# Kernel tuning notes

Measured on AMD Instinct MI355X. Metric: run time of the kernel, lower is better.

The kernel has to match this reference:

```python
import jax, jax.numpy as jnp
import numpy as np

KAPPA = 0.1
U0 = 1.0
LATT = (32, 32, 32, 32)  # (Lx, Ly, Lz, Lt)


def _gamma_matrices(dtype=jnp.complex64):
    g = np.zeros((4, 4, 4), dtype=np.complex64)
    g[0] = np.array([[0, 0, 0, 1j], [0, 0, 1j, 0], [0, -1j, 0, 0], [-1j, 0, 0, 0]])
    g[1] = np.array([[0, 0, 0, -1], [0, 0, 1, 0], [0, 1, 0, 0], [-1, 0, 0, 0]])
    g[2] = np.array([[0, 0, 1j, 0], [0, 0, 0, -1j], [-1j, 0, 0, 0], [0, 1j, 0, 0]])
    g[3] = np.array([[0, 0, 1, 0], [0, 0, 0, 1], [1, 0, 0, 0], [0, 1, 0, 0]])
    return jnp.asarray(g, dtype=dtype)


def setup_inputs() -> dict:
    key = jax.random.key(0)
    k1, k2, k3, k4 = jax.random.split(key, 4)
    Lx, Ly, Lz, Lt = LATT
    src_shape = (4, 3, Lt, Lz, Ly, Lx)        # [s, c, t, z, y, x]
    U_shape = (3, 3, 4, Lt, Lz, Ly, Lx)       # [C, c, d, t, z, y, x]
    return {
        "src_re": jax.random.normal(k1, src_shape, dtype=jnp.float32),
        "src_im": jax.random.normal(k2, src_shape, dtype=jnp.float32),
        "U_re": jax.random.normal(k3, U_shape, dtype=jnp.float32),
        "U_im": jax.random.normal(k4, U_shape, dtype=jnp.float32),
    }


def _wilson(src, U, kappa=KAPPA, u_0=U0):
    """Wilson-Dirac operator: dest = src - kappa/u0 * sum_mu hopping terms.
    src: [s,c,t,z,y,x] complex; U: [C,c,d,t,z,y,x] complex."""
    gamma = _gamma_matrices(src.dtype)
    I4 = jnp.eye(4, dtype=src.dtype)
    U_dag = jnp.conj(jnp.swapaxes(U, 0, 1))  # dagger on color indices
    dest = src
    for mu in range(4):
        axis = -1 - mu  # mu=0 -> x axis (-1), ..., mu=3 -> t axis (-4)
        U_mu = U[:, :, mu]            # [C,c,t,z,y,x]
        U_dag_mu = U_dag[:, :, mu]
        # forward hop: (1 - gamma_mu) U_mu src(x+mu)
        src_plus = jnp.roll(src, -1, axis)
        term1 = jnp.einsum('Ss,Cctzyx,sctzyx->SCtzyx', I4 - gamma[mu], U_mu, src_plus)
        # backward hop: (1 + gamma_mu) U_dag(x-mu) src(x-mu)
        src_minus = jnp.roll(src, 1, axis)
        U_dag_minus = jnp.roll(U_dag_mu, 1, axis)
        term2 = jnp.einsum('Ss,Cctzyx,sctzyx->SCtzyx', I4 + gamma[mu], U_dag_minus, src_minus)
        dest = dest - (kappa / u_0) * (term1 + term2)
    return dest


def reference(src_re, src_im, U_re, U_im):
    src = jax.lax.complex(src_re, src_im)
    U = jax.lax.complex(U_re, U_im)
    return _wilson(src, U)
```

## Files before the change

kernel.cpp:

```cpp
#include <hip/hip_runtime.h>

constexpr int VOL = 32 * 32 * 32 * 32;
constexpr float KAPPA = 0.1f;
constexpr int TSTEP = 4;

struct alignas(8) F2 { float x, y; };
using f2v = __attribute__((ext_vector_type(2))) float;

__device__ __forceinline__ F2 operator+(F2 a, F2 b) { return F2{a.x + b.x, a.y + b.y}; }
__device__ __forceinline__ F2 operator-(F2 a, F2 b) { return F2{a.x - b.x, a.y - b.y}; }
__device__ __forceinline__ F2 operator*(F2 a, F2 b) { return F2{a.x * b.x, a.y * b.y}; }
__device__ __forceinline__ F2 operator*(float s, F2 a) { return F2{s * a.x, s * a.y}; }

__device__ __forceinline__ F2 ld2(const float* __restrict__ p, int idx) {
    return *reinterpret_cast<const F2*>(p + idx);
}
__device__ __forceinline__ void st_nt2(float* __restrict__ p, F2 v) {
    f2v t = {v.x, v.y};
    __builtin_nontemporal_store(t, reinterpret_cast<f2v*>(p));
}

struct Direct {
    const float* re; const float* im; int site;
    __device__ __forceinline__ void load(int s, int c, F2& r, F2& i) const {
        int idx = (s * 3 + c) * VOL + site;
        r = ld2(re, idx); i = ld2(im, idx);
    }
};
struct SRegs {
    const F2* r; const F2* i;
    __device__ __forceinline__ void load(int s, int c, F2& rr, F2& ii) const {
        rr = r[s * 3 + c]; ii = i[s * 3 + c];
    }
};
struct LDSDirect {
    const float (*L)[512]; int q;
    __device__ __forceinline__ void load(int s, int c, F2& r, F2& i) const {
        int k = (s * 3 + c) * 2;
        r = *reinterpret_cast<const F2*>(&L[k][q]);
        i = *reinterpret_cast<const F2*>(&L[k + 1][q]);
    }
};
struct LDSShift {
    const float (*L)[512]; int i0, i1;
    __device__ __forceinline__ void load(int s, int c, F2& r, F2& i) const {
        int k = (s * 3 + c) * 2;
        r = F2{L[k][i0], L[k][i1]};
        i = F2{L[k + 1][i0], L[k + 1][i1]};
    }
};

struct UDirect {
    const float* re; const float* im; int mu, site;
    __device__ __forceinline__ void load(int a, int b, F2& r, F2& i) const {
        int idx = ((a * 3 + b) * 4 + mu) * VOL + site;
        r = ld2(re, idx); i = ld2(im, idx);
    }
};
struct URegs {
    const F2* r; const F2* i;
    __device__ __forceinline__ void load(int a, int b, F2& rr, F2& ii) const {
        rr = r[a * 3 + b]; ii = i[a * 3 + b];
    }
};
struct UShiftRegs {
    const F2* cr; const F2* ci; const float* blr; const float* bli;
    __device__ __forceinline__ void load(int a, int b, F2& rr, F2& ii) const {
        int e = a * 3 + b;
        rr = F2{blr[e], cr[e].x};
        ii = F2{bli[e], ci[e].x};
    }
};

template <int MU, int S, class SL, class UL>
__device__ __forceinline__ void hop(const SL& sl, const UL& ul, F2 dr[4][3]) {
    constexpr bool DAG = (S < 0);
    constexpr bool NEEDI = (MU == 0 || MU == 2);
    const float s = (float)S;

    F2 hr[2][3], hi[2][3];
#pragma unroll
    for (int c = 0; c < 3; ++c) {
        F2 p0r, p0i, p1r, p1i, p2r, p2i, p3r, p3i;
        sl.load(0, c, p0r, p0i);
        sl.load(1, c, p1r, p1i);
        sl.load(2, c, p2r, p2i);
        sl.load(3, c, p3r, p3i);
        if (MU == 0) {
            hr[0][c] = p0r + s * p3i;  hi[0][c] = p0i - s * p3r;
            hr[1][c] = p1r + s * p2i;  hi[1][c] = p1i - s * p2r;
        } else if (MU == 1) {
            hr[0][c] = p0r + s * p3r;  hi[0][c] = p0i + s * p3i;
            hr[1][c] = p1r - s * p2r;  hi[1][c] = p1i - s * p2i;
        } else if (MU == 2) {
            hr[0][c] = p0r + s * p2i;  hi[0][c] = p0i - s * p2r;
            hr[1][c] = p1r - s * p3i;  hi[1][c] = p1i + s * p3r;
        } else {
            hr[0][c] = p0r - s * p2r;  hi[0][c] = p0i - s * p2i;
            hr[1][c] = p1r - s * p3r;  hi[1][c] = p1i - s * p3i;
        }
    }

    const float k = KAPPA, ks = KAPPA * s;
#pragma unroll
    for (int a = 0; a < 3; ++a) {
        F2 wr[3], wi[3];
#pragma unroll
        for (int b = 0; b < 3; ++b) {
            F2 r, i;
            if (DAG) { ul.load(b, a, r, i); wi[b] = F2{-i.x, -i.y}; }
            else     { ul.load(a, b, r, i); wi[b] = i; }
            wr[b] = r;
        }
        F2 ar0{0,0}, ar1{0,0}, ai0{0,0}, ai1{0,0};
#pragma unroll
        for (int b = 0; b < 3; ++b) {
            ar0 = ar0 + wr[b] * hr[0][b] - wi[b] * hi[0][b];
            ar1 = ar1 + wr[b] * hr[1][b] - wi[b] * hi[1][b];
            if (NEEDI) {
                ai0 = ai0 + wr[b] * hi[0][b] + wi[b] * hr[0][b];
                ai1 = ai1 + wr[b] * hi[1][b] + wi[b] * hr[1][b];
            }
        }
        dr[0][a] = dr[0][a] - k * ar0;
        dr[1][a] = dr[1][a] - k * ar1;
        if (MU == 0)      { dr[2][a] = dr[2][a] + ks * ai1; dr[3][a] = dr[3][a] + ks * ai0; }
        else if (MU == 1) { dr[2][a] = dr[2][a] + ks * ar1; dr[3][a] = dr[3][a] - ks * ar0; }
        else if (MU == 2) { dr[2][a] = dr[2][a] + ks * ai0; dr[3][a] = dr[3][a] - ks * ai1; }
        else              { dr[2][a] = dr[2][a] + ks * ar0; dr[3][a] = dr[3][a] + ks * ar1; }
    }
}

__global__ __launch_bounds__(256)
void wilson_kernel(const float* __restrict__ src_re, const float* __restrict__ src_im,
                   const float* __restrict__ U_re, const float* __restrict__ U_im,
                   float* __restrict__ out) {
    __shared__ float lds[24][512];

    int b = blockIdx.x;
    int xcd = b & 7;
    int loc = b >> 3;
    int h = loc & 1;
    int z = loc >> 1;
    int t0 = xcd << 2;

    int q  = threadIdx.x * 2;
    int lx = q & 31, ly = q >> 5;
    int y  = (h << 4) | ly;
    int base = (((z << 5) | y) << 5) | lx;

    int row = ly * 32;
    int iR0 = row + ((lx + 1) & 31), iR1 = row + ((lx + 2) & 31);
    int iL0 = row + ((lx + 31) & 31);

    int s0  = (t0 << 15) | base;
    int sm1 = (((t0 + 31) & 31) << 15) | base;
    F2 dr[4][3];
#pragma unroll
    for (int k = 0; k < 12; ++k) {
        F2 r = ld2(src_re, k * VOL + s0);
        F2 i = ld2(src_im, k * VOL + s0);
        *reinterpret_cast<F2*>(&lds[2 * k][q])     = r;
        *reinterpret_cast<F2*>(&lds[2 * k + 1][q]) = i;
        dr[k / 3][k % 3] = r;
    }
    hop<3, -1>(Direct{src_re, src_im, sm1}, UDirect{U_re, U_im, 3, sm1}, dr);
    __syncthreads();

#pragma unroll
    for (int i = 0; i < TSTEP; ++i) {
        int t = t0 + i;
        int s = (t << 15) | base;
        int snext = (((t + 1) & 31) << 15) | base;

        {
            int gxm1 = (s & ~31) | ((lx + 31) & 31);
            F2 uxr[9], uxi[9];
            float blr[9], bli[9];
#pragma unroll
            for (int e = 0; e < 9; ++e) {
                uxr[e] = ld2(U_re, (e * 4 + 0) * VOL + s);
                uxi[e] = ld2(U_im, (e * 4 + 0) * VOL + s);
                blr[e] = U_re[(e * 4 + 0) * VOL + gxm1];
                bli[e] = U_im[(e * 4 + 0) * VOL + gxm1];
            }
            hop<0,  1>(LDSShift{lds, iR0, iR1}, URegs{uxr, uxi}, dr);
            hop<0, -1>(LDSShift{lds, iL0, q},   UShiftRegs{uxr, uxi, blr, bli}, dr);
        }

        {
            int syp = (s & ~(31 << 5)) | (((y + 1)  & 31) << 5);
            int sym = (s & ~(31 << 5)) | (((y + 31) & 31) << 5);
            if (ly < 15) hop<1,  1>(LDSDirect{lds, q + 32}, UDirect{U_re, U_im, 1, s}, dr);
            else         hop<1,  1>(Direct{src_re, src_im, syp}, UDirect{U_re, U_im, 1, s}, dr);
            if (ly > 0)  hop<1, -1>(LDSDirect{lds, q - 32}, UDirect{U_re, U_im, 1, sym}, dr);
            else         hop<1, -1>(Direct{src_re, src_im, sym}, UDirect{U_re, U_im, 1, sym}, dr);
        }

        {
            int szp = (s & ~(31 << 10)) | (((z + 1)  & 31) << 10);
            int szm = (s & ~(31 << 10)) | (((z + 31) & 31) << 10);
            hop<2,  1>(Direct{src_re, src_im, szp}, UDirect{U_re, U_im, 2, s}, dr);
            hop<2, -1>(Direct{src_re, src_im, szm}, UDirect{U_re, U_im, 2, szm}, dr);
        }

        F2 nr[12], ni[12];
#pragma unroll
        for (int k = 0; k < 12; ++k) {
            nr[k] = ld2(src_re, k * VOL + snext);
            ni[k] = ld2(src_im, k * VOL + snext);
        }
        F2 utr[9], uti[9];
#pragma unroll
        for (int e = 0; e < 9; ++e) {
            utr[e] = ld2(U_re, (e * 4 + 3) * VOL + s);
            uti[e] = ld2(U_im, (e * 4 + 3) * VOL + s);
        }

        hop<3,  1>(SRegs{nr, ni}, URegs{utr, uti}, dr);
#pragma unroll
        for (int ss = 0; ss < 4; ++ss)
#pragma unroll
            for (int c = 0; c < 3; ++c)
                st_nt2(out + (ss * 3 + c) * VOL + s, dr[ss][c]);

        if (i < TSTEP - 1) {
#pragma unroll
            for (int k = 0; k < 12; ++k) dr[k / 3][k % 3] = nr[k];
            hop<3, -1>(LDSDirect{lds, q}, URegs{utr, uti}, dr);
            __syncthreads();
#pragma unroll
            for (int k = 0; k < 12; ++k) {
                *reinterpret_cast<F2*>(&lds[2 * k][q])     = nr[k];
                *reinterpret_cast<F2*>(&lds[2 * k + 1][q]) = ni[k];
            }
            __syncthreads();
        }
    }
}

extern "C" void kernel_launch(void* const* d_in, const int* in_sizes, int n_in,
                              void* d_out, int out_size, void* d_ws, size_t ws_size,
                              hipStream_t stream) {
    const float* src_re = (const float*)d_in[0];
    const float* src_im = (const float*)d_in[1];
    const float* U_re   = (const float*)d_in[2];
    const float* U_im   = (const float*)d_in[3];
    float* out = (float*)d_out;

    dim3 block(256);
    dim3 grid(VOL / 2 / 256 / TSTEP);
    wilson_kernel<<<grid, block, 0, stream>>>(src_re, src_im, U_re, U_im, out);
}
```

Baseline: 142.7 us.

## Retile block to 2z×8y slab and share x/y backward links via shuffles

Changes each block's tile from a 16-row y half-plane to a 2(z)×8(y)×32(x) slab, so z-neighbour spinors come from LDS for one of the two z hops. The x-backward gauge link is now taken from a neighbouring lane with a cross-lane shuffle instead of a separate global load. The y-backward link is likewise shuffled from the lane 16 below, with a global load only for lanes on the tile edge. This aims to cut global/L2 traffic for halo data, at the cost of more y-boundary global loads, since the y tile is smaller, and extra shuffle and register pressure.

```diff
diff --git a/kernel.cpp b/kernel.cpp
--- a/kernel.cpp
+++ b/kernel.cpp
@@ -140,18 +140,26 @@
     int b = blockIdx.x;
     int xcd = b & 7;
     int loc = b >> 3;
-    int h = loc & 1;
-    int z = loc >> 1;
+    int zp = loc & 15;
+    int yq = loc >> 4;
+    int z0 = zp << 1;
+    int y0 = yq << 3;
     int t0 = xcd << 2;
 
-    int q  = threadIdx.x * 2;
-    int lx = q & 31, ly = q >> 5;
-    int y  = (h << 4) | ly;
-    int base = (((z << 5) | y) << 5) | lx;
-
-    int row = ly * 32;
-    int iR0 = row + ((lx + 1) & 31), iR1 = row + ((lx + 2) & 31);
-    int iL0 = row + ((lx + 31) & 31);
+    int tid = threadIdx.x;
+    int lane = tid & 63;
+    int q  = tid * 2;
+    int lx = q & 31;
+    int ly = (q >> 5) & 7;
+    int lz = q >> 8;
+    int y = y0 + ly;
+    int z = z0 + lz;
+    int base = ((z << 10) | (y << 5)) | lx;
+
+    int rowq = q & ~31;
+    int iR0 = rowq | ((lx + 1) & 31), iR1 = rowq | ((lx + 2) & 31);
+    int iL0 = rowq | ((lx + 31) & 31);
+    int rot = (lane & ~15) | ((lane + 15) & 15);
 
     int s0  = (t0 << 15) | base;
     int sm1 = (((t0 + 31) & 31) << 15) | base;
@@ -174,15 +182,17 @@
         int snext = (((t + 1) & 31) << 15) | base;
 
         {
-            int gxm1 = (s & ~31) | ((lx + 31) & 31);
             F2 uxr[9], uxi[9];
             float blr[9], bli[9];
 #pragma unroll
             for (int e = 0; e < 9; ++e) {
                 uxr[e] = ld2(U_re, (e * 4 + 0) * VOL + s);
                 uxi[e] = ld2(U_im, (e * 4 + 0) * VOL + s);
-                blr[e] = U_re[(e * 4 + 0) * VOL + gxm1];
-                bli[e] = U_im[(e * 4 + 0) * VOL + gxm1];
+            }
+#pragma unroll
+            for (int e = 0; e < 9; ++e) {
+                blr[e] = __shfl(uxr[e].y, rot);
+                bli[e] = __shfl(uxi[e].y, rot);
             }
             hop<0,  1>(LDSShift{lds, iR0, iR1}, URegs{uxr, uxi}, dr);
             hop<0, -1>(LDSShift{lds, iL0, q},   UShiftRegs{uxr, uxi, blr, bli}, dr);
@@ -191,17 +201,41 @@
         {
             int syp = (s & ~(31 << 5)) | (((y + 1)  & 31) << 5);
             int sym = (s & ~(31 << 5)) | (((y + 31) & 31) << 5);
-            if (ly < 15) hop<1,  1>(LDSDirect{lds, q + 32}, UDirect{U_re, U_im, 1, s}, dr);
-            else         hop<1,  1>(Direct{src_re, src_im, syp}, UDirect{U_re, U_im, 1, s}, dr);
-            if (ly > 0)  hop<1, -1>(LDSDirect{lds, q - 32}, UDirect{U_re, U_im, 1, sym}, dr);
-            else         hop<1, -1>(Direct{src_re, src_im, sym}, UDirect{U_re, U_im, 1, sym}, dr);
+            F2 uyr[9], uyi[9];
+#pragma unroll
+            for (int e = 0; e < 9; ++e) {
+                uyr[e] = ld2(U_re, (e * 4 + 1) * VOL + s);
+                uyi[e] = ld2(U_im, (e * 4 + 1) * VOL + s);
+            }
+            F2 ubr[9], ubi[9];
+#pragma unroll
+            for (int e = 0; e < 9; ++e) {
+                ubr[e] = F2{__shfl(uyr[e].x, lane - 16), __shfl(uyr[e].y, lane - 16)};
+                ubi[e] = F2{__shfl(uyi[e].x, lane - 16), __shfl(uyi[e].y, lane - 16)};
+            }
+            if (lane < 16) {
+#pragma unroll
+                for (int e = 0; e < 9; ++e) {
+                    ubr[e] = ld2(U_re, (e * 4 + 1) * VOL + sym);
+                    ubi[e] = ld2(U_im, (e * 4 + 1) * VOL + sym);
+                }
+            }
+            if (ly < 7) hop<1,  1>(LDSDirect{lds, q + 32}, URegs{uyr, uyi}, dr);
+            else        hop<1,  1>(Direct{src_re, src_im, syp}, URegs{uyr, uyi}, dr);
+            if (ly > 0) hop<1, -1>(LDSDirect{lds, q - 32}, URegs{ubr, ubi}, dr);
+            else        hop<1, -1>(Direct{src_re, src_im, sym}, URegs{ubr, ubi}, dr);
         }
 
         {
             int szp = (s & ~(31 << 10)) | (((z + 1)  & 31) << 10);
             int szm = (s & ~(31 << 10)) | (((z + 31) & 31) << 10);
-            hop<2,  1>(Direct{src_re, src_im, szp}, UDirect{U_re, U_im, 2, s}, dr);
-            hop<2, -1>(Direct{src_re, src_im, szm}, UDirect{U_re, U_im, 2, szm}, dr);
+            if (lz == 0) {
+                hop<2,  1>(LDSDirect{lds, q + 256}, UDirect{U_re, U_im, 2, s}, dr);
+                hop<2, -1>(Direct{src_re, src_im, szm}, UDirect{U_re, U_im, 2, szm}, dr);
+            } else {
+                hop<2,  1>(Direct{src_re, src_im, szp}, UDirect{U_re, U_im, 2, s}, dr);
+                hop<2, -1>(LDSDirect{lds, q - 256}, UDirect{U_re, U_im, 2, szm}, dr);
+            }
         }
 
         F2 nr[12], ni[12];
```

After: 150.0 us. 1.05x slower.
